# Performance work log

Measured on AMD Instinct MI355X. Metric: run time of the kernel, lower is better.

## Reference

```python
import jax, jax.numpy as jnp
import numpy as np


def conv1x1(x, w, b):
    # x: [B,C,H,W], w: [O,C], b: [O]
    return jnp.einsum('bchw,oc->bohw', x, w) + b[None, :, None, None]


def resize_bilinear(x, h, w):
    # matches torch F.interpolate(mode='bilinear', align_corners=False), no antialias
    B, C = x.shape[:2]
    return jax.image.resize(x, (B, C, h, w), method='bilinear', antialias=False)


def attend(q_map, k_map, v_map, num_heads, scale):
    # q_map/k_map/v_map: [B, hidden, H, W] -> out [B, hidden, H, W]
    B, D, H, W = q_map.shape
    hd = D // num_heads
    N = H * W
    q = q_map.reshape(B, num_heads, hd, N).transpose(0, 1, 3, 2)  # [B,h,N,d]
    k = k_map.reshape(B, num_heads, hd, N)                         # [B,h,d,N]
    v = v_map.reshape(B, num_heads, hd, N).transpose(0, 1, 3, 2)  # [B,h,N,d]
    scores = jnp.einsum('bhnd,bhdm->bhnm', q, k) * scale
    attn = jax.nn.softmax(scores, axis=-1)
    out = jnp.einsum('bhnm,bhmd->bhnd', attn, v)                   # [B,h,N,d]
    return out.transpose(0, 1, 3, 2).reshape(B, D, H, W)


NUM_HEADS = 8
HIDDEN = 256
HEAD_DIM = HIDDEN // NUM_HEADS
SCALE = HEAD_DIM ** -0.5


def setup_inputs() -> dict:
    key = jax.random.key(0)
    ks = jax.random.split(key, 20)
    C_h, C_l = 128, 256
    inp = {
        'high_feat': jax.random.normal(ks[0], (2, C_h, 64, 64), jnp.float32),
        'low_feat': jax.random.normal(ks[1], (2, C_l, 32, 32), jnp.float32),
    }
    def lin(k, o, c):
        kw, kb = jax.random.split(k)
        s = 1.0 / np.sqrt(c)
        return (jax.random.uniform(kw, (o, c), jnp.float32, -s, s),
                jax.random.uniform(kb, (o,), jnp.float32, -s, s))
    inp['q_high_w'], inp['q_high_b'] = lin(ks[2], HIDDEN, C_h)
    inp['k_high_w'], inp['k_high_b'] = lin(ks[3], HIDDEN, C_h)
    inp['v_high_w'], inp['v_high_b'] = lin(ks[4], HIDDEN, C_h)
    inp['q_low_w'], inp['q_low_b'] = lin(ks[5], HIDDEN, C_l)
    inp['k_low_w'], inp['k_low_b'] = lin(ks[6], HIDDEN, C_l)
    inp['v_low_w'], inp['v_low_b'] = lin(ks[7], HIDDEN, C_l)
    inp['out_high_w'], inp['out_high_b'] = lin(ks[8], C_h, HIDDEN)
    inp['out_low_w'], inp['out_low_b'] = lin(ks[9], C_l, HIDDEN)
    return inp


def reference(high_feat, low_feat,
              q_high_w, q_high_b, k_high_w, k_high_b, v_high_w, v_high_b,
              q_low_w, q_low_b, k_low_w, k_low_b, v_low_w, v_low_b,
              out_high_w, out_high_b, out_low_w, out_low_b):
    B, C_h, H, W = high_feat.shape
    _, C_l, Hl, Wl = low_feat.shape

    # high queries attend to upsampled-low keys/values
    low_up = resize_bilinear(low_feat, H, W)
    q_h = conv1x1(high_feat, q_high_w, q_high_b)
    k_l = conv1x1(low_up, k_low_w, k_low_b)
    v_l = conv1x1(low_up, v_low_w, v_low_b)
    high_out = attend(q_h, k_l, v_l, NUM_HEADS, SCALE)
    high_out = conv1x1(high_out, out_high_w, out_high_b)

    # low queries attend to downsampled-high keys/values
    q_l = conv1x1(low_feat, q_low_w, q_low_b)
    k_h = resize_bilinear(conv1x1(high_feat, k_high_w, k_high_b), Hl, Wl)
    v_h = resize_bilinear(conv1x1(high_feat, v_high_w, v_high_b), Hl, Wl)
    low_out = attend(q_l, k_h, v_h, NUM_HEADS, SCALE)
    low_out = conv1x1(low_out, out_low_w, out_low_b)

    return (high_out, low_out)
```

## Files before the change

### kernel.cpp

```cpp
#include <hip/hip_runtime.h>
#include <hip/hip_bf16.h>

#define HEADS 8
#define HD    32

typedef __attribute__((ext_vector_type(8))) short short8;
typedef __attribute__((ext_vector_type(4))) float f32x4;
typedef unsigned short us;

__device__ __forceinline__ us f2bf(float f) {
  union { __hip_bfloat16 h; us u; } cv;
  cv.h = __float2bfloat16(f);
  return cv.u;
}
__device__ __forceinline__ float bf2f(us u) {
  union { float f; unsigned int i; } cv;
  cv.i = ((unsigned int)u) << 16;
  return cv.f;
}
__device__ __forceinline__ float exp2_native(float x) {
  float r;
  asm("v_exp_f32 %0, %1" : "=v"(r) : "v"(x));
  return r;
}
__device__ __forceinline__ void glds16(const us* g, us* l) {
  __builtin_amdgcn_global_load_lds(
      (const __attribute__((address_space(1))) void*)g,
      (__attribute__((address_space(3))) void*)l, 16, 0, 0);
}

struct GP {
  const void* X; const float* W; const float* bias; void* out;
  int C, O, N, omode; float alpha;
};

template<int XMODE>
__global__ __launch_bounds__(256) void gemm_conv(
    GP g0, GP g1, GP g2, GP g3, int nb0, int nb1, int nb2) {
  __shared__ __align__(16) us Wh[2][64 * 32], Wl[2][64 * 32];
  __shared__ __align__(16) us Xh[2][64 * 32], Xl[2][64 * 32];
  int bid = blockIdx.x;
  GP g;
  if (bid < nb0) g = g0;
  else if (bid < nb0 + nb1) { g = g1; bid -= nb0; }
  else if (bid < nb0 + nb1 + nb2) { g = g2; bid -= nb0 + nb1; }
  else { g = g3; bid -= nb0 + nb1 + nb2; }
  const int C = g.C, O = g.O, N = g.N;
  int nx = N >> 6, nyo = O >> 6;
  int b = bid / (nx * nyo);
  int rr = bid - b * (nx * nyo);
  int o0 = (rr / nx) << 6;
  int n0 = (rr - (rr / nx) * nx) << 6;

  int tid = threadIdx.x, w = tid >> 6, l = tid & 63, lq = l & 15, l4 = l >> 4;

  int wr = tid >> 2, wcb = tid & 3;
  int xn = tid & 63, xcg = tid >> 6;
  const float* Wp = g.W + (size_t)(o0 + wr) * C + wcb * 8;
  const float* Xf = (const float*)g.X;
  const unsigned int* Xp = (const unsigned int*)g.X;
  size_t xbase = (size_t)b * C * N + n0 + xn;
  int wof = wr * 32 + ((wcb ^ ((wr >> 1) & 3)) << 3);
  int xof = xn * 32 + ((xcg ^ ((xn >> 1) & 3)) << 3);

  auto stage = [&](int s, int bufi) {
    int c0 = s << 5;
    float4 wa = *(const float4*)(Wp + c0);
    float4 wb = *(const float4*)(Wp + c0 + 4);
    float wv[8] = {wa.x, wa.y, wa.z, wa.w, wb.x, wb.y, wb.z, wb.w};
    short8 whv, wlv;
#pragma unroll
    for (int j = 0; j < 8; ++j) {
      us h = f2bf(wv[j]);
      whv[j] = (short)h;
      wlv[j] = (short)f2bf(wv[j] - bf2f(h));
    }
    *(short8*)&Wh[bufi][wof] = whv;
    *(short8*)&Wl[bufi][wof] = wlv;
    short8 xhv, xlv;
#pragma unroll
    for (int j = 0; j < 8; ++j) {
      int c = c0 + xcg * 8 + j;
      if constexpr (XMODE == 0) {
        float xv = Xf[xbase + (size_t)c * N];
        us h = f2bf(xv);
        xhv[j] = (short)h;
        xlv[j] = (short)f2bf(xv - bf2f(h));
      } else {
        unsigned int xv = Xp[xbase + (size_t)c * N];
        xhv[j] = (short)(xv >> 16);
        xlv[j] = (short)(xv & 0xffffu);
      }
    }
    *(short8*)&Xh[bufi][xof] = xhv;
    *(short8*)&Xl[bufi][xof] = xlv;
  };

  f32x4 acc[4] = {{0,0,0,0},{0,0,0,0},{0,0,0,0},{0,0,0,0}};
  int ns = C >> 5, cur = 0;
  stage(0, 0);
  for (int s = 0; s < ns; ++s) {
    __syncthreads();
    if (s + 1 < ns) stage(s + 1, cur ^ 1);
    int swz = (l4 ^ ((lq >> 1) & 3)) << 3;
    int arow = w * 16 + lq;
    short8 ah = *(const short8*)&Wh[cur][arow * 32 + swz];
    short8 al = *(const short8*)&Wl[cur][arow * 32 + swz];
    __builtin_amdgcn_s_setprio(1);
#pragma unroll
    for (int nf = 0; nf < 4; ++nf) {
      int brow = nf * 16 + lq;
      short8 bh = *(const short8*)&Xh[cur][brow * 32 + swz];
      short8 bl = *(const short8*)&Xl[cur][brow * 32 + swz];
      acc[nf] = __builtin_amdgcn_mfma_f32_16x16x32_bf16(ah, bh, acc[nf], 0, 0, 0);
      acc[nf] = __builtin_amdgcn_mfma_f32_16x16x32_bf16(ah, bl, acc[nf], 0, 0, 0);
      acc[nf] = __builtin_amdgcn_mfma_f32_16x16x32_bf16(al, bh, acc[nf], 0, 0, 0);
    }
    __builtin_amdgcn_s_setprio(0);
    cur ^= 1;
  }

  float bv[4];
#pragma unroll
  for (int r = 0; r < 4; ++r) bv[r] = g.bias[o0 + w * 16 + l4 * 4 + r];
  if (g.omode == 0) {
    us* ob = (us*)g.out;
#pragma unroll
    for (int nf = 0; nf < 4; ++nf) {
      ushort4 pk;
      pk.x = f2bf((acc[nf][0] + bv[0]) * g.alpha);
      pk.y = f2bf((acc[nf][1] + bv[1]) * g.alpha);
      pk.z = f2bf((acc[nf][2] + bv[2]) * g.alpha);
      pk.w = f2bf((acc[nf][3] + bv[3]) * g.alpha);
      *(ushort4*)&ob[((size_t)b * N + n0 + nf * 16 + lq) * O + o0 + w * 16 + l4 * 4] = pk;
    }
  } else if (g.omode == 1) {
    us* ob = (us*)g.out;
#pragma unroll
    for (int nf = 0; nf < 4; ++nf)
#pragma unroll
      for (int r = 0; r < 4; ++r)
        ob[((size_t)(b * O + o0 + w * 16 + l4 * 4 + r)) * N + n0 + nf * 16 + lq] =
            f2bf(acc[nf][r] + bv[r]);
  } else {
    float* of = (float*)g.out;
#pragma unroll
    for (int nf = 0; nf < 4; ++nf)
#pragma unroll
      for (int r = 0; r < 4; ++r)
        of[((size_t)(b * O + o0 + w * 16 + l4 * 4 + r)) * N + n0 + nf * 16 + lq] =
            acc[nf][r] + bv[r];
  }
}

__global__ __launch_bounds__(256) void upsample_both(
    const us* __restrict__ inT, us* __restrict__ outT,
    const us* __restrict__ inC, us* __restrict__ outC, int nbT, int BC) {
  if ((int)blockIdx.x < nbT) {
    int rowg = blockIdx.x * 4 + (threadIdx.x >> 6);
    int ch = (threadIdx.x & 63) * 4;
    int b = rowg >> 12, n = rowg & 4095;
    int y = n >> 6, x = n & 63;
    float sy = y * 0.5f - 0.25f, sx = x * 0.5f - 0.25f;
    int y0 = (int)floorf(sy), x0 = (int)floorf(sx);
    float fy = sy - (float)y0, fx = sx - (float)x0;
    int y0c = max(y0, 0), y1c = min(y0 + 1, 31);
    int x0c = max(x0, 0), x1c = min(x0 + 1, 31);
    const us* ip = inT + (size_t)b * 1024 * 256 + ch;
    ushort4 v00 = *(const ushort4*)&ip[(size_t)(y0c * 32 + x0c) * 256];
    ushort4 v01 = *(const ushort4*)&ip[(size_t)(y0c * 32 + x1c) * 256];
    ushort4 v10 = *(const ushort4*)&ip[(size_t)(y1c * 32 + x0c) * 256];
    ushort4 v11 = *(const ushort4*)&ip[(size_t)(y1c * 32 + x1c) * 256];
    float w00 = (1.f - fy) * (1.f - fx), w01 = (1.f - fy) * fx;
    float w10 = fy * (1.f - fx), w11 = fy * fx;
    ushort4 o;
    o.x = f2bf(w00 * bf2f(v00.x) + w01 * bf2f(v01.x) + w10 * bf2f(v10.x) + w11 * bf2f(v11.x));
    o.y = f2bf(w00 * bf2f(v00.y) + w01 * bf2f(v01.y) + w10 * bf2f(v10.y) + w11 * bf2f(v11.y));
    o.z = f2bf(w00 * bf2f(v00.z) + w01 * bf2f(v01.z) + w10 * bf2f(v10.z) + w11 * bf2f(v11.z));
    o.w = f2bf(w00 * bf2f(v00.w) + w01 * bf2f(v01.w) + w10 * bf2f(v10.w) + w11 * bf2f(v11.w));
    *(ushort4*)&outT[((size_t)b * 4096 + n) * 256 + ch] = o;
  } else {
    int t = ((int)blockIdx.x - nbT) * 256 + threadIdx.x;
    if (t >= BC * 64) return;
    int y = t & 63, bc = t >> 6;
    float sy = y * 0.5f - 0.25f;
    int y0 = (int)floorf(sy);
    float fy = sy - (float)y0;
    int y0c = max(y0, 0), y1c = min(y0 + 1, 31);
    const us* r0 = inC + (size_t)bc * 1024 + y0c * 32;
    const us* r1 = inC + (size_t)bc * 1024 + y1c * 32;
    float m[32];
#pragma unroll
    for (int j = 0; j < 32; j += 8) {
      short8 a = *(const short8*)(r0 + j);
      short8 c = *(const short8*)(r1 + j);
#pragma unroll
      for (int e = 0; e < 8; ++e)
        m[j + e] = (1.f - fy) * bf2f((us)a[e]) + fy * bf2f((us)c[e]);
    }
    us* op = outC + (size_t)bc * 4096 + y * 64;
    short8 o8;
#pragma unroll
    for (int xo = 0; xo < 64; ++xo) {
      int k = xo >> 1;
      float v;
      if (xo & 1) v = (k < 31) ? 0.75f * m[k] + 0.25f * m[k + 1] : m[31];
      else        v = (k > 0) ? 0.25f * m[k - 1] + 0.75f * m[k] : m[0];
      o8[xo & 7] = (short)f2bf(v);
      if ((xo & 7) == 7) *(short8*)(op + (xo & ~7)) = o8;
    }
  }
}

__global__ __launch_bounds__(256) void downsample_pack_k(
    const float* __restrict__ in, unsigned int* __restrict__ opk, int BC) {
  int t = blockIdx.x * 256 + threadIdx.x;
  if (t >= BC * 1024) return;
  int x = t & 31, y = (t >> 5) & 31, bc = t >> 10;
  const float* ip = in + (size_t)bc * 4096 + (y * 2) * 64 + x * 2;
  float v = 0.25f * (ip[0] + ip[1] + ip[64] + ip[65]);
  us h = f2bf(v);
  opk[t] = ((unsigned int)h << 16) | f2bf(v - bf2f(h));
}

__global__ __launch_bounds__(256) void attn_mfma(
    const us* __restrict__ qT0, const us* __restrict__ kT0,
    const us* __restrict__ vC0, unsigned int* __restrict__ o0,
    int N0, int nb0,
    const us* __restrict__ qT1, const us* __restrict__ kT1,
    const us* __restrict__ vC1, unsigned int* __restrict__ o1,
    int N1) {
  __shared__ __align__(16) us Kt[2][64 * 32];
  __shared__ __align__(16) us Vt[2][32 * 64];
  __shared__ __align__(16) us Pt[4][16 * 64];

  int bid = blockIdx.x;
  const us *qT, *kT, *vC; unsigned int* opk; int N, bh, qb;
  if (bid < nb0) {
    qT = qT0; kT = kT0; vC = vC0; opk = o0; N = N0;
    int xcd = bid & 7, slot = bid >> 3, nqb = N0 >> 6;
    qb = slot & (nqb - 1);
    bh = ((slot / nqb) << 3) | xcd;
  } else {
    bid -= nb0;
    qT = qT1; kT = kT1; vC = vC1; opk = o1; N = N1;
    int xcd = bid & 7, slot = bid >> 3, nqb = N1 >> 6;
    qb = slot & (nqb - 1);
    bh = ((slot / nqb) << 3) | xcd;
  }
  int b = bh >> 3, h = bh & 7;
  int tid = threadIdx.x;
  int w = tid >> 6, l = tid & 63;
  int lq = l & 15, l4 = l >> 4;

  short8 qfrag;
  {
    const us* qp =
        qT + ((size_t)(b * N + qb * 64 + w * 16 + lq)) * 256 + h * 32 + l4 * 8;
    qfrag = *(const short8*)qp;
  }

  int rK = w * 16 + (l >> 2);
  const us* gK = kT + ((size_t)(b * N + rK)) * 256 + h * 32 +
                 (((l & 3) ^ ((rK >> 1) & 3)) << 3);
  int dV = w * 8 + (l >> 3);
  const us* gV = vC + ((size_t)(b * 256 + h * 32 + dV)) * N +
                 (((l & 7) ^ (dV & 7)) << 3);

  f32x4 acc0 = {0.f, 0.f, 0.f, 0.f}, acc1 = {0.f, 0.f, 0.f, 0.f};
  f32x4 acc2 = {0.f, 0.f, 0.f, 0.f};
  short8 ones;
#pragma unroll
  for (int j = 0; j < 8; ++j) ones[j] = (short)0x3F80;
  us* Pw = Pt[w];

  glds16(gK, &Kt[0][w * 512]);
  glds16(gV, &Vt[0][w * 512]);

  int nt = N >> 6, cur = 0;
  for (int t = 0; t < nt; ++t) {
    __syncthreads();
    if (t + 1 < nt) {
      glds16(gK + (size_t)(t + 1) * 64 * 256, &Kt[cur ^ 1][w * 512]);
      glds16(gV + (t + 1) * 64, &Vt[cur ^ 1][w * 512]);
    }
    const us* Kb = Kt[cur];
    const us* Vb = Vt[cur];

#pragma unroll
    for (int kg = 0; kg < 4; ++kg) {
      int key = kg * 16 + lq;
      short8 a = *(const short8*)&Kb[key * 32 + ((l4 ^ ((key >> 1) & 3)) << 3)];
      f32x4 zero = {0.f, 0.f, 0.f, 0.f};
      __builtin_amdgcn_s_setprio(1);
      f32x4 s = __builtin_amdgcn_mfma_f32_16x16x32_bf16(a, qfrag, zero, 0, 0, 0);
      __builtin_amdgcn_s_setprio(0);
      float p0 = exp2_native(s[0]);
      float p1 = exp2_native(s[1]);
      float p2 = exp2_native(s[2]);
      float p3 = exp2_native(s[3]);
      unsigned int r01, r23;
      asm("v_cvt_pk_bf16_f32 %0, %1, %2" : "=v"(r01) : "v"(p0), "v"(p1));
      asm("v_cvt_pk_bf16_f32 %0, %1, %2" : "=v"(r23) : "v"(p2), "v"(p3));
      uint2 pk; pk.x = r01; pk.y = r23;
      int key0 = kg * 16 + l4 * 4;
      *(uint2*)&Pw[lq * 64 + (((key0 >> 3) ^ (lq & 7)) << 3) + (key0 & 7)] = pk;
    }

#pragma unroll
    for (int kh = 0; kh < 2; ++kh) {
      short8 pfr = *(const short8*)&Pw[lq * 64 + (((kh * 4 + l4) ^ (lq & 7)) << 3)];
      int d0 = lq, d1 = 16 + lq;
      short8 vf0 = *(const short8*)&Vb[d0 * 64 + (((kh * 4 + l4) ^ (d0 & 7)) << 3)];
      short8 vf1 = *(const short8*)&Vb[d1 * 64 + (((kh * 4 + l4) ^ (d1 & 7)) << 3)];
      __builtin_amdgcn_s_setprio(1);
      acc0 = __builtin_amdgcn_mfma_f32_16x16x32_bf16(vf0, pfr, acc0, 0, 0, 0);
      acc1 = __builtin_amdgcn_mfma_f32_16x16x32_bf16(vf1, pfr, acc1, 0, 0, 0);
      acc2 = __builtin_amdgcn_mfma_f32_16x16x32_bf16(ones, pfr, acc2, 0, 0, 0);
      __builtin_amdgcn_s_setprio(0);
    }
    cur ^= 1;
  }

  float inv = 1.f / acc2[0];

  unsigned int* op = opk + ((size_t)(b * 256 + h * 32)) * N + qb * 64 + w * 16 + lq;
#pragma unroll
  for (int r = 0; r < 4; ++r) {
    float v0 = acc0[r] * inv;
    us h0 = f2bf(v0);
    op[(size_t)(l4 * 4 + r) * N] = ((unsigned int)h0 << 16) | f2bf(v0 - bf2f(h0));
    float v1 = acc1[r] * inv;
    us h1 = f2bf(v1);
    op[(size_t)(16 + l4 * 4 + r) * N] = ((unsigned int)h1 << 16) | f2bf(v1 - bf2f(h1));
  }
}

extern "C" void kernel_launch(void* const* d_in, const int* in_sizes, int n_in,
                              void* d_out, int out_size, void* d_ws, size_t ws_size,
                              hipStream_t stream) {
  const float* high_feat  = (const float*)d_in[0];
  const float* low_feat   = (const float*)d_in[1];
  const float* q_high_w   = (const float*)d_in[2];
  const float* q_high_b   = (const float*)d_in[3];
  const float* k_high_w   = (const float*)d_in[4];
  const float* k_high_b   = (const float*)d_in[5];
  const float* v_high_w   = (const float*)d_in[6];
  const float* v_high_b   = (const float*)d_in[7];
  const float* q_low_w    = (const float*)d_in[8];
  const float* q_low_b    = (const float*)d_in[9];
  const float* k_low_w    = (const float*)d_in[10];
  const float* k_low_b    = (const float*)d_in[11];
  const float* v_low_w    = (const float*)d_in[12];
  const float* v_low_b    = (const float*)d_in[13];
  const float* out_high_w = (const float*)d_in[14];
  const float* out_high_b = (const float*)d_in[15];
  const float* out_low_w  = (const float*)d_in[16];
  const float* out_low_b  = (const float*)d_in[17];

  const int B = 2, Nh = 4096, Nl = 1024;
  const float qa = 0.17677669529663689f * 1.4426950408889634f;

  char* p = (char*)d_ws;
  us* qT    = (us*)p; p += (size_t)2 * 4096 * 256 * 2;
  us* kTb   = (us*)p; p += (size_t)2 * 4096 * 256 * 2;
  us* vCb   = (us*)p; p += (size_t)2 * 256 * 4096 * 2;
  us* klbT  = (us*)p; p += (size_t)2 * 1024 * 256 * 2;
  us* vlb   = (us*)p; p += (size_t)2 * 256 * 1024 * 2;
  unsigned int* aoh  = (unsigned int*)p; p += (size_t)2 * 256 * 4096 * 4;
  unsigned int* hfdn = (unsigned int*)p; p += (size_t)2 * 128 * 1024 * 4;
  us* qTl   = (us*)p; p += (size_t)2 * 1024 * 256 * 2;
  us* kTl   = (us*)p; p += (size_t)2 * 1024 * 256 * 2;
  us* vCl   = (us*)p; p += (size_t)2 * 256 * 1024 * 2;
  unsigned int* aol  = (unsigned int*)p; p += (size_t)2 * 256 * 1024 * 4;

  float* out_high = (float*)d_out;
  float* out_low  = out_high + 2 * 128 * 4096;

  downsample_pack_k<<<(B * 128 * 1024) / 256, 256, 0, stream>>>(high_feat, hfdn, B * 128);

  {
    GP s0 = {low_feat,  k_low_w,  k_low_b,  klbT, 256, 256, Nl, 0, 1.0f};
    GP s1 = {low_feat,  v_low_w,  v_low_b,  vlb,  256, 256, Nl, 1, 1.0f};
    GP s2 = {high_feat, q_high_w, q_high_b, qT,   128, 256, Nh, 0, qa};
    GP s3 = {low_feat,  q_low_w,  q_low_b,  qTl,  256, 256, Nl, 0, qa};
    gemm_conv<0><<<896, 256, 0, stream>>>(s0, s1, s2, s3, 128, 128, 512);
  }
  upsample_both<<<2048 + 128, 256, 0, stream>>>(klbT, kTb, vlb, vCb, 2048, B * 256);
  {
    GP s0 = {hfdn, k_high_w, k_high_b, kTl, 128, 256, Nl, 0, 1.0f};
    GP s1 = {hfdn, v_high_w, v_high_b, vCl, 128, 256, Nl, 1, 1.0f};
    gemm_conv<1><<<256, 256, 0, stream>>>(s0, s1, s0, s0, 128, 128, 0);
  }
  attn_mfma<<<16 * (Nh / 64) + 16 * (Nl / 64), 256, 0, stream>>>(
      qT, kTb, vCb, aoh, Nh, 16 * (Nh / 64),
      qTl, kTl, vCl, aol, Nl);
  {
    GP s0 = {aoh, out_high_w, out_high_b, out_high, 256, 128, Nh, 2, 1.0f};
    GP s1 = {aol, out_low_w,  out_low_b,  out_low,  256, 256, Nl, 2, 1.0f};
    gemm_conv<1><<<384, 256, 0, stream>>>(s0, s1, s0, s0, 256, 128, 0);
  }
}
```

Baseline: 120.9 us.

## Process two query groups per attention block to reuse K/V tiles

Each attention block now handles 128 queries instead of 64: every wave holds two Q fragments and two sets of accumulators, and the P scratch in shared memory doubles. Each K/V tile loaded into LDS is used for twice the query work, which halves K/V global traffic and the number of blocks. In exchange it raises register and LDS use per block and halves the grid, which may lower occupancy and load balance, particularly for the smaller low-resolution attention.

Measured after the change: 125.6 us. 1.04x slower.

```diff
diff --git a/kernel.cpp b/kernel.cpp
--- a/kernel.cpp
+++ b/kernel.cpp
@@ -232,19 +232,19 @@
     int N1) {
   __shared__ __align__(16) us Kt[2][64 * 32];
   __shared__ __align__(16) us Vt[2][32 * 64];
-  __shared__ __align__(16) us Pt[4][16 * 64];
+  __shared__ __align__(16) us Pt[8][16 * 64];
 
   int bid = blockIdx.x;
   const us *qT, *kT, *vC; unsigned int* opk; int N, bh, qb;
   if (bid < nb0) {
     qT = qT0; kT = kT0; vC = vC0; opk = o0; N = N0;
-    int xcd = bid & 7, slot = bid >> 3, nqb = N0 >> 6;
+    int xcd = bid & 7, slot = bid >> 3, nqb = N0 >> 7;
     qb = slot & (nqb - 1);
     bh = ((slot / nqb) << 3) | xcd;
   } else {
     bid -= nb0;
     qT = qT1; kT = kT1; vC = vC1; opk = o1; N = N1;
-    int xcd = bid & 7, slot = bid >> 3, nqb = N1 >> 6;
+    int xcd = bid & 7, slot = bid >> 3, nqb = N1 >> 7;
     qb = slot & (nqb - 1);
     bh = ((slot / nqb) << 3) | xcd;
   }
@@ -253,11 +253,12 @@
   int w = tid >> 6, l = tid & 63;
   int lq = l & 15, l4 = l >> 4;
 
-  short8 qfrag;
-  {
-    const us* qp =
-        qT + ((size_t)(b * N + qb * 64 + w * 16 + lq)) * 256 + h * 32 + l4 * 8;
-    qfrag = *(const short8*)qp;
+  short8 qfrag[2];
+#pragma unroll
+  for (int g = 0; g < 2; ++g) {
+    const us* qp = qT + ((size_t)(b * N + qb * 128 + g * 64 + w * 16 + lq)) * 256 +
+                   h * 32 + l4 * 8;
+    qfrag[g] = *(const short8*)qp;
   }
 
   int rK = w * 16 + (l >> 2);
@@ -267,12 +268,12 @@
   const us* gV = vC + ((size_t)(b * 256 + h * 32 + dV)) * N +
                  (((l & 7) ^ (dV & 7)) << 3);
 
-  f32x4 acc0 = {0.f, 0.f, 0.f, 0.f}, acc1 = {0.f, 0.f, 0.f, 0.f};
-  f32x4 acc2 = {0.f, 0.f, 0.f, 0.f};
+  f32x4 acc0[2] = {{0,0,0,0},{0,0,0,0}};
+  f32x4 acc1[2] = {{0,0,0,0},{0,0,0,0}};
+  f32x4 acc2[2] = {{0,0,0,0},{0,0,0,0}};
   short8 ones;
 #pragma unroll
   for (int j = 0; j < 8; ++j) ones[j] = (short)0x3F80;
-  us* Pw = Pt[w];
 
   glds16(gK, &Kt[0][w * 512]);
   glds16(gV, &Vt[0][w * 512]);
@@ -292,47 +293,58 @@
       int key = kg * 16 + lq;
       short8 a = *(const short8*)&Kb[key * 32 + ((l4 ^ ((key >> 1) & 3)) << 3)];
       f32x4 zero = {0.f, 0.f, 0.f, 0.f};
-      __builtin_amdgcn_s_setprio(1);
-      f32x4 s = __builtin_amdgcn_mfma_f32_16x16x32_bf16(a, qfrag, zero, 0, 0, 0);
-      __builtin_amdgcn_s_setprio(0);
-      float p0 = exp2_native(s[0]);
-      float p1 = exp2_native(s[1]);
-      float p2 = exp2_native(s[2]);
-      float p3 = exp2_native(s[3]);
-      unsigned int r01, r23;
-      asm("v_cvt_pk_bf16_f32 %0, %1, %2" : "=v"(r01) : "v"(p0), "v"(p1));
-      asm("v_cvt_pk_bf16_f32 %0, %1, %2" : "=v"(r23) : "v"(p2), "v"(p3));
-      uint2 pk; pk.x = r01; pk.y = r23;
       int key0 = kg * 16 + l4 * 4;
-      *(uint2*)&Pw[lq * 64 + (((key0 >> 3) ^ (lq & 7)) << 3) + (key0 & 7)] = pk;
+      int pof = lq * 64 + (((key0 >> 3) ^ (lq & 7)) << 3) + (key0 & 7);
+#pragma unroll
+      for (int g = 0; g < 2; ++g) {
+        __builtin_amdgcn_s_setprio(1);
+        f32x4 s = __builtin_amdgcn_mfma_f32_16x16x32_bf16(a, qfrag[g], zero, 0, 0, 0);
+        __builtin_amdgcn_s_setprio(0);
+        float p0 = exp2_native(s[0]);
+        float p1 = exp2_native(s[1]);
+        float p2 = exp2_native(s[2]);
+        float p3 = exp2_native(s[3]);
+        unsigned int r01, r23;
+        asm("v_cvt_pk_bf16_f32 %0, %1, %2" : "=v"(r01) : "v"(p0), "v"(p1));
+        asm("v_cvt_pk_bf16_f32 %0, %1, %2" : "=v"(r23) : "v"(p2), "v"(p3));
+        uint2 pk; pk.x = r01; pk.y = r23;
+        *(uint2*)&Pt[w * 2 + g][pof] = pk;
+      }
     }
 
 #pragma unroll
     for (int kh = 0; kh < 2; ++kh) {
-      short8 pfr = *(const short8*)&Pw[lq * 64 + (((kh * 4 + l4) ^ (lq & 7)) << 3)];
       int d0 = lq, d1 = 16 + lq;
       short8 vf0 = *(const short8*)&Vb[d0 * 64 + (((kh * 4 + l4) ^ (d0 & 7)) << 3)];
       short8 vf1 = *(const short8*)&Vb[d1 * 64 + (((kh * 4 + l4) ^ (d1 & 7)) << 3)];
-      __builtin_amdgcn_s_setprio(1);
-      acc0 = __builtin_amdgcn_mfma_f32_16x16x32_bf16(vf0, pfr, acc0, 0, 0, 0);
-      acc1 = __builtin_amdgcn_mfma_f32_16x16x32_bf16(vf1, pfr, acc1, 0, 0, 0);
-      acc2 = __builtin_amdgcn_mfma_f32_16x16x32_bf16(ones, pfr, acc2, 0, 0, 0);
-      __builtin_amdgcn_s_setprio(0);
+      int pof = lq * 64 + (((kh * 4 + l4) ^ (lq & 7)) << 3);
+#pragma unroll
+      for (int g = 0; g < 2; ++g) {
+        short8 pfr = *(const short8*)&Pt[w * 2 + g][pof];
+        __builtin_amdgcn_s_setprio(1);
+        acc0[g] = __builtin_amdgcn_mfma_f32_16x16x32_bf16(vf0, pfr, acc0[g], 0, 0, 0);
+        acc1[g] = __builtin_amdgcn_mfma_f32_16x16x32_bf16(vf1, pfr, acc1[g], 0, 0, 0);
+        acc2[g] = __builtin_amdgcn_mfma_f32_16x16x32_bf16(ones, pfr, acc2[g], 0, 0, 0);
+        __builtin_amdgcn_s_setprio(0);
+      }
     }
     cur ^= 1;
   }
 
-  float inv = 1.f / acc2[0];
-
-  unsigned int* op = opk + ((size_t)(b * 256 + h * 32)) * N + qb * 64 + w * 16 + lq;
-#pragma unroll
-  for (int r = 0; r < 4; ++r) {
-    float v0 = acc0[r] * inv;
-    us h0 = f2bf(v0);
-    op[(size_t)(l4 * 4 + r) * N] = ((unsigned int)h0 << 16) | f2bf(v0 - bf2f(h0));
-    float v1 = acc1[r] * inv;
-    us h1 = f2bf(v1);
-    op[(size_t)(16 + l4 * 4 + r) * N] = ((unsigned int)h1 << 16) | f2bf(v1 - bf2f(h1));
+#pragma unroll
+  for (int g = 0; g < 2; ++g) {
+    float inv = 1.f / acc2[g][0];
+    unsigned int* op = opk + ((size_t)(b * 256 + h * 32)) * N +
+                       qb * 128 + g * 64 + w * 16 + lq;
+#pragma unroll
+    for (int r = 0; r < 4; ++r) {
+      float v0 = acc0[g][r] * inv;
+      us h0 = f2bf(v0);
+      op[(size_t)(l4 * 4 + r) * N] = ((unsigned int)h0 << 16) | f2bf(v0 - bf2f(h0));
+      float v1 = acc1[g][r] * inv;
+      us h1 = f2bf(v1);
+      op[(size_t)(16 + l4 * 4 + r) * N] = ((unsigned int)h1 << 16) | f2bf(v1 - bf2f(h1));
+    }
   }
 }
 
@@ -392,8 +404,8 @@
     GP s1 = {hfdn, v_high_w, v_high_b, vCl, 128, 256, Nl, 1, 1.0f};
     gemm_conv<1><<<256, 256, 0, stream>>>(s0, s1, s0, s0, 128, 128, 0);
   }
-  attn_mfma<<<16 * (Nh / 64) + 16 * (Nl / 64), 256, 0, stream>>>(
-      qT, kTb, vCb, aoh, Nh, 16 * (Nh / 64),
+  attn_mfma<<<16 * (Nh / 128) + 16 * (Nl / 128), 256, 0, stream>>>(
+      qT, kTb, vCb, aoh, Nh, 16 * (Nh / 128),
       qTl, kTl, vCl, aol, Nl);
   {
     GP s0 = {aoh, out_high_w, out_high_b, out_high, 256, 128, Nh, 2, 1.0f};
```
